# Kernel tuning notes

Hardware: AMD Instinct MI355X
Metric: run time of the kernel (lower is better)

Reference implementation:

```python
import jax, jax.numpy as jnp
import numpy as np

N_NODES = 50000
N_EDGES = 800000
IN_CH = 128
OUT_CH = 32
HEADS = 4
NEG_SLOPE = 0.2


def setup_inputs() -> dict:
    key = jax.random.key(0)
    k_feat, k_src, k_dst, k_w, k_a = jax.random.split(key, 5)
    feat = jax.random.normal(k_feat, (N_NODES, IN_CH), dtype=jnp.float32)
    src = jax.random.randint(k_src, (N_EDGES,), 0, N_NODES, dtype=jnp.int64)
    dst = jax.random.randint(k_dst, (N_EDGES,), 0, N_NODES, dtype=jnp.int64)
    # forward removes self-loops then re-adds them; build inputs with no self-loops
    dst = jnp.where(src == dst, (dst + 1) % N_NODES, dst)
    edge_index = jnp.stack([src, dst])  # [2, E]
    # glorot init, matching reset_parameters
    def glorot(k, shape):
        stdv = np.sqrt(6.0 / (shape[-2] + shape[-1]))
        return jax.random.uniform(k, shape, jnp.float32, -stdv, stdv)
    weight = glorot(k_w, (IN_CH, HEADS * OUT_CH))
    att = glorot(k_a, (1, HEADS, 2 * OUT_CH))
    bias = jnp.zeros((HEADS * OUT_CH,), dtype=jnp.float32)
    return {"feat": feat, "edge_index": edge_index, "weight": weight, "att": att, "bias": bias}


def reference(feat, edge_index, weight, att, bias):
    N = feat.shape[0]
    # add self-loops (inputs are constructed self-loop free)
    loop = jnp.arange(N, dtype=edge_index.dtype)
    ei = jnp.concatenate([edge_index, jnp.stack([loop, loop])], axis=1)
    src, dst = ei[0], ei[1]

    x = (feat @ weight).reshape(N, HEADS, OUT_CH)  # [N,H,C]
    x_i = x[dst]  # dst features, [E,H,C]
    x_j = x[src]  # src features, [E,H,C]

    # GAT attention: sum over concat([x_i, x_j]) * att
    alpha = jnp.sum(jnp.concatenate([x_i, x_j], axis=-1) * att, axis=-1)  # [E,H]
    alpha = jax.nn.leaky_relu(alpha, NEG_SLOPE)

    # scatter softmax normalized per src node (edge_index[0]), as in the original code
    amax = jax.ops.segment_max(alpha, src, num_segments=N)  # every node is a src (self-loops)
    amax = jax.lax.stop_gradient(amax)
    ex = jnp.exp(alpha - amax[src])
    esum = jax.ops.segment_sum(ex, src, num_segments=N)
    alpha = ex / (esum[src] + 1e-16)  # [E,H]

    neighbor = x_j * alpha[:, :, None]  # [E,H,C]
    out = jax.ops.segment_sum(neighbor, dst, num_segments=N)  # sum-aggregate into dst
    out = out.reshape(N, HEADS * OUT_CH) + bias  # concat heads + bias
    return out
```

## Files before the change

### kernel.cpp

```cpp
#include <hip/hip_runtime.h>
#include <hip/hip_bf16.h>

#define N_NODES 50000
#define E_EDGES 800000
#define ET (E_EDGES + N_NODES)
#define HEADS 4
#define HC 128
#define NEG_SLOPE 0.2f
#define SCAN_B 256
#define NBLK ((N_NODES + SCAN_B - 1) / SCAN_B)

__device__ __forceinline__ unsigned short f2bf(float f) {
    unsigned u = __float_as_uint(f);
    unsigned r = u + 0x7FFFu + ((u >> 16) & 1u);
    return (unsigned short)(r >> 16);
}

__global__ __launch_bounds__(256)
void gemm_kernel(const float* __restrict__ feat, const float* __restrict__ weight,
                 const float* __restrict__ att,
                 unsigned short* __restrict__ xb,
                 float* __restrict__ a_i, float* __restrict__ a_j)
{
    __shared__ float sA[32][68];
    __shared__ float sB[32][132];
    const int t = threadIdx.x;
    const int row0 = blockIdx.x * 64;
    const int rg = t >> 4;
    const int cg = t & 15;

    float acc[4][8];
#pragma unroll
    for (int i = 0; i < 4; i++)
#pragma unroll
        for (int j = 0; j < 8; j++) acc[i][j] = 0.f;

    for (int kc = 0; kc < 128; kc += 32) {
        __syncthreads();
#pragma unroll
        for (int q = 0; q < 2; q++) {
            int qi = t + q * 256;
            int row = qi >> 3;
            int kq = qi & 7;
            int grow = row0 + row;
            float4 v = make_float4(0.f, 0.f, 0.f, 0.f);
            if (grow < N_NODES)
                v = *(const float4*)&feat[grow * 128 + kc + kq * 4];
            sA[kq * 4 + 0][row] = v.x; sA[kq * 4 + 1][row] = v.y;
            sA[kq * 4 + 2][row] = v.z; sA[kq * 4 + 3][row] = v.w;
        }
#pragma unroll
        for (int q = 0; q < 4; q++) {
            int qi = t + q * 256;
            int k = qi >> 5;
            int cq = qi & 31;
            float4 v = *(const float4*)&weight[(kc + k) * 128 + cq * 4];
            *(float4*)&sB[k][cq * 4] = v;
        }
        __syncthreads();
#pragma unroll 4
        for (int k = 0; k < 32; k++) {
            float4 a0 = *(const float4*)&sA[k][4 * rg];
            float4 b0 = *(const float4*)&sB[k][4 * cg];
            float4 b1 = *(const float4*)&sB[k][64 + 4 * cg];
#define FMA_ROW(r, ar) \
            acc[r][0] = fmaf(ar, b0.x, acc[r][0]); \
            acc[r][1] = fmaf(ar, b0.y, acc[r][1]); \
            acc[r][2] = fmaf(ar, b0.z, acc[r][2]); \
            acc[r][3] = fmaf(ar, b0.w, acc[r][3]); \
            acc[r][4] = fmaf(ar, b1.x, acc[r][4]); \
            acc[r][5] = fmaf(ar, b1.y, acc[r][5]); \
            acc[r][6] = fmaf(ar, b1.z, acc[r][6]); \
            acc[r][7] = fmaf(ar, b1.w, acc[r][7]);
            FMA_ROW(0, a0.x)
            FMA_ROW(1, a0.y)
            FMA_ROW(2, a0.z)
            FMA_ROW(3, a0.w)
#undef FMA_ROW
        }
    }

    const int h0 = cg >> 3;
    const int cih = (4 * cg) & 31;
    float ai_c[2][4], aj_c[2][4];
#pragma unroll
    for (int g = 0; g < 2; g++) {
        int h = h0 + g * 2;
#pragma unroll
        for (int j = 0; j < 4; j++) {
            ai_c[g][j] = att[h * 64 + cih + j];
            aj_c[g][j] = att[h * 64 + 32 + cih + j];
        }
    }
#pragma unroll
    for (int i = 0; i < 4; i++) {
        int row = row0 + 4 * rg + i;
        if (row >= N_NODES) continue;
        unsigned p0 = (unsigned)f2bf(acc[i][0]) | ((unsigned)f2bf(acc[i][1]) << 16);
        unsigned p1 = (unsigned)f2bf(acc[i][2]) | ((unsigned)f2bf(acc[i][3]) << 16);
        unsigned p2 = (unsigned)f2bf(acc[i][4]) | ((unsigned)f2bf(acc[i][5]) << 16);
        unsigned p3 = (unsigned)f2bf(acc[i][6]) | ((unsigned)f2bf(acc[i][7]) << 16);
        uint2 q0; q0.x = p0; q0.y = p1;
        uint2 q1; q1.x = p2; q1.y = p3;
        *(uint2*)&xb[row * 128 + 4 * cg] = q0;
        *(uint2*)&xb[row * 128 + 64 + 4 * cg] = q1;

        float pi0 = 0.f, pj0 = 0.f, pi1 = 0.f, pj1 = 0.f;
#pragma unroll
        for (int j = 0; j < 4; j++) {
            pi0 = fmaf(acc[i][j], ai_c[0][j], pi0);
            pj0 = fmaf(acc[i][j], aj_c[0][j], pj0);
            pi1 = fmaf(acc[i][4 + j], ai_c[1][j], pi1);
            pj1 = fmaf(acc[i][4 + j], aj_c[1][j], pj1);
        }
#pragma unroll
        for (int m = 1; m <= 4; m <<= 1) {
            pi0 += __shfl_xor(pi0, m, 64);
            pj0 += __shfl_xor(pj0, m, 64);
            pi1 += __shfl_xor(pi1, m, 64);
            pj1 += __shfl_xor(pj1, m, 64);
        }
        if ((cg & 7) == 0) {
            a_i[row * 4 + h0]     = pi0;
            a_i[row * 4 + h0 + 2] = pi1;
            a_j[row * 4 + h0]     = pj0;
            a_j[row * 4 + h0 + 2] = pj1;
        }
    }
}

__global__ __launch_bounds__(256)
void rank_pass(const int* __restrict__ ei, int* __restrict__ deg_s,
               int* __restrict__ deg_d, unsigned short* __restrict__ rank_s,
               unsigned short* __restrict__ rank_d)
{
    int e = blockIdx.x * 256 + threadIdx.x;
    if (e >= ET) return;
    int s, d;
    if (e < E_EDGES) { s = ei[e]; d = ei[E_EDGES + e]; }
    else { s = d = e - E_EDGES; }
    rank_s[e] = (unsigned short)atomicAdd(&deg_s[s], 1);
    rank_d[e] = (unsigned short)atomicAdd(&deg_d[d], 1);
}

__global__ __launch_bounds__(SCAN_B)
void partial_kernel(const int* __restrict__ deg_s, const int* __restrict__ deg_d,
                    int* __restrict__ partials)
{
    __shared__ int wsum[4];
    int half = (blockIdx.x < NBLK) ? 0 : 1;
    int blk = half ? (blockIdx.x - NBLK) : blockIdx.x;
    const int* deg = half ? deg_d : deg_s;
    int idx = blk * SCAN_B + threadIdx.x;
    int v = (idx < N_NODES) ? deg[idx] : 0;
#pragma unroll
    for (int m = 1; m < 64; m <<= 1) v += __shfl_xor(v, m, 64);
    int lane = threadIdx.x & 63, wid = threadIdx.x >> 6;
    if (lane == 0) wsum[wid] = v;
    __syncthreads();
    if (threadIdx.x == 0)
        partials[blockIdx.x] = wsum[0] + wsum[1] + wsum[2] + wsum[3];
}

__global__ __launch_bounds__(512)
void scanp_kernel(int* __restrict__ partials, int* __restrict__ off_s,
                  int* __restrict__ off_d)
{
    __shared__ int sh[512];
    int t = threadIdx.x;
    int hf = t & 255;
    int v = 0;
    if (t < 256)      v = (hf < NBLK) ? partials[hf] : 0;
    else              v = (hf < NBLK) ? partials[NBLK + hf] : 0;
    sh[t] = v;
    __syncthreads();
    for (int dlt = 1; dlt < 256; dlt <<= 1) {
        int u = (hf >= dlt) ? sh[t - dlt] : 0;
        __syncthreads();
        sh[t] += u;
        __syncthreads();
    }
    int excl = (hf == 0) ? 0 : sh[t - 1];
    if (t < 256) { if (hf < NBLK) partials[hf] = excl; }
    else         { if (hf < NBLK) partials[NBLK + hf] = excl; }
    if (t == NBLK - 1)       off_s[N_NODES] = sh[t];
    if (t == 256 + NBLK - 1) off_d[N_NODES] = sh[t];
}

__global__ __launch_bounds__(SCAN_B)
void final_kernel(const int* __restrict__ deg_s, const int* __restrict__ deg_d,
                  const int* __restrict__ partials,
                  int* __restrict__ off_s, int* __restrict__ off_d)
{
    __shared__ int wsum[4];
    int half = (blockIdx.x < NBLK) ? 0 : 1;
    int blk = half ? (blockIdx.x - NBLK) : blockIdx.x;
    const int* deg = half ? deg_d : deg_s;
    int* off = half ? off_d : off_s;
    int idx = blk * SCAN_B + threadIdx.x;
    int val = (idx < N_NODES) ? deg[idx] : 0;
    int lane = threadIdx.x & 63, wid = threadIdx.x >> 6;
    int x = val;
#pragma unroll
    for (int dlt = 1; dlt < 64; dlt <<= 1) {
        int y = __shfl_up(x, dlt, 64);
        if (lane >= dlt) x += y;
    }
    if (lane == 63) wsum[wid] = x;
    __syncthreads();
    int woff = 0;
    for (int w = 0; w < wid; w++) woff += wsum[w];
    int excl = x - val + woff + partials[blockIdx.x];
    if (idx < N_NODES) off[idx] = excl;
}

__global__ __launch_bounds__(256)
void place_kernel(const int* __restrict__ ei, const int* __restrict__ off_s,
                  const int* __restrict__ off_d,
                  const unsigned short* __restrict__ rank_s,
                  const unsigned short* __restrict__ rank_d,
                  int* __restrict__ adj_dst, int* __restrict__ adj_src)
{
    int e = blockIdx.x * 256 + threadIdx.x;
    if (e >= ET) return;
    int s, d;
    if (e < E_EDGES) { s = ei[e]; d = ei[E_EDGES + e]; }
    else { s = d = e - E_EDGES; }
    adj_dst[off_s[s] + rank_s[e]] = d;
    adj_src[off_d[d] + rank_d[e]] = s;
}

__global__ __launch_bounds__(256)
void esum_kernel(const int* __restrict__ off_s, const int* __restrict__ adj_dst,
                 const float* __restrict__ a_i, const float* __restrict__ a_j,
                 float* __restrict__ esum)
{
    int tid = blockIdx.x * 256 + threadIdx.x;
    int node = tid >> 2;
    if (node >= N_NODES) return;
    int h = tid & 3;
    int start = off_s[node], end = off_s[node + 1];
    float ajh = a_j[node * 4 + h];
    float acc = 0.f;
    int s_cur[4];
#pragma unroll
    for (int k = 0; k < 4; k++)
        s_cur[k] = (start + k < end) ? adj_dst[start + k] : 0;
    for (int i0 = start; i0 < end; i0 += 4) {
        int i1 = i0 + 4;
        int s_nxt[4];
#pragma unroll
        for (int k = 0; k < 4; k++)
            s_nxt[k] = (i1 + k < end) ? adj_dst[i1 + k] : 0;
        float aiv[4];
#pragma unroll
        for (int k = 0; k < 4; k++)
            aiv[k] = a_i[s_cur[k] * 4 + h];
#pragma unroll
        for (int k = 0; k < 4; k++) {
            if (i0 + k < end) {
                float al = aiv[k] + ajh;
                al = al > 0.f ? al : NEG_SLOPE * al;
                acc += __expf(al);
            }
        }
#pragma unroll
        for (int k = 0; k < 4; k++) s_cur[k] = s_nxt[k];
    }
    esum[node * 4 + h] = acc;
}

__global__ __launch_bounds__(256)
void coef_kernel(const int* __restrict__ off_d, const int* __restrict__ adj_src,
                 const float* __restrict__ a_i, const float* __restrict__ a_j,
                 const float* __restrict__ esum, float* __restrict__ coef)
{
    int tid = blockIdx.x * 256 + threadIdx.x;
    int node = tid >> 2;
    if (node >= N_NODES) return;
    int h = tid & 3;
    int start = off_d[node], end = off_d[node + 1];
    float aih = a_i[node * 4 + h];
    int s_cur[4];
#pragma unroll
    for (int k = 0; k < 4; k++)
        s_cur[k] = (start + k < end) ? adj_src[start + k] : 0;
    for (int i0 = start; i0 < end; i0 += 4) {
        int i1 = i0 + 4;
        int s_nxt[4];
#pragma unroll
        for (int k = 0; k < 4; k++)
            s_nxt[k] = (i1 + k < end) ? adj_src[i1 + k] : 0;
        float ajv[4], esv[4];
#pragma unroll
        for (int k = 0; k < 4; k++) {
            ajv[k] = a_j[s_cur[k] * 4 + h];
            esv[k] = esum[s_cur[k] * 4 + h];
        }
#pragma unroll
        for (int k = 0; k < 4; k++) {
            if (i0 + k < end) {
                float al = aih + ajv[k];
                al = al > 0.f ? al : NEG_SLOPE * al;
                coef[(i0 + k) * 4 + h] = __expf(al) / (esv[k] + 1e-16f);
            }
        }
#pragma unroll
        for (int k = 0; k < 4; k++) s_cur[k] = s_nxt[k];
    }
}

__global__ __launch_bounds__(256)
void aggregate(const int* __restrict__ off, const int* __restrict__ srcsorted,
               const float* __restrict__ coef, const unsigned* __restrict__ xb32,
               const float* __restrict__ bias, float* __restrict__ out)
{
    int node = blockIdx.x * 4 + (threadIdx.x >> 6);
    if (node >= N_NODES) return;
    int lane = threadIdx.x & 63;
    int h = lane >> 4;
    int start = off[node], end = off[node + 1];
    float acc0 = 0.f, acc1 = 0.f;

    int s_cur[4]; float c_cur[4];
#pragma unroll
    for (int k = 0; k < 4; k++) {
        bool v = (start + k < end);
        s_cur[k] = v ? srcsorted[start + k] : 0;
        c_cur[k] = v ? coef[(start + k) * 4 + h] : 0.f;
    }
    for (int i0 = start; i0 < end; i0 += 4) {
        int i1 = i0 + 4;
        int s_nxt[4]; float c_nxt[4];
#pragma unroll
        for (int k = 0; k < 4; k++) {
            bool v = (i1 + k < end);
            s_nxt[k] = v ? srcsorted[i1 + k] : 0;
            c_nxt[k] = v ? coef[(i1 + k) * 4 + h] : 0.f;
        }
        unsigned xp[4];
#pragma unroll
        for (int k = 0; k < 4; k++)
            xp[k] = xb32[s_cur[k] * 64 + lane];
#pragma unroll
        for (int k = 0; k < 4; k++) {
            float x0 = __uint_as_float(xp[k] << 16);
            float x1 = __uint_as_float(xp[k] & 0xFFFF0000u);
            acc0 = fmaf(x0, c_cur[k], acc0);
            acc1 = fmaf(x1, c_cur[k], acc1);
        }
#pragma unroll
        for (int k = 0; k < 4; k++) { s_cur[k] = s_nxt[k]; c_cur[k] = c_nxt[k]; }
    }
    float2 o;
    o.x = acc0 + bias[2 * lane];
    o.y = acc1 + bias[2 * lane + 1];
    *(float2*)&out[node * 128 + 2 * lane] = o;
}

extern "C" void kernel_launch(void* const* d_in, const int* in_sizes, int n_in,
                              void* d_out, int out_size, void* d_ws, size_t ws_size,
                              hipStream_t stream)
{
    const float* feat   = (const float*)d_in[0];
    const int*   ei     = (const int*)d_in[1];
    const float* weight = (const float*)d_in[2];
    const float* att    = (const float*)d_in[3];
    const float* bias   = (const float*)d_in[4];
    float* out = (float*)d_out;
    char* ws = (char*)d_ws;

    unsigned short* rank_s = (unsigned short*)ws;
    unsigned short* rank_d = (unsigned short*)(ws + 1700000);
    unsigned short* xb = (unsigned short*)ws;
    float* a_i   = (float*)(ws + 12800000);
    float* a_j   = (float*)(ws + 13600000);
    float* esum  = (float*)(ws + 14400000);
    int*   deg_s = (int*)(ws + 15200000);
    int*   deg_d = (int*)(ws + 15400000);
    int*   off_s = (int*)(ws + 15600000);
    int*   off_d = (int*)(ws + 15800016);
    int*   adj_dst = (int*)(ws + 16000032);
    int*   adj_src = (int*)(ws + 19400032);
    int*   partials = (int*)(ws + 22800032);
    float* coef  = (float*)(ws + 22801600);

    hipMemsetAsync(ws + 15200000, 0, 400000, stream);

    rank_pass<<<(ET + 255) / 256, 256, 0, stream>>>(ei, deg_s, deg_d, rank_s, rank_d);
    partial_kernel<<<2 * NBLK, SCAN_B, 0, stream>>>(deg_s, deg_d, partials);
    scanp_kernel<<<1, 512, 0, stream>>>(partials, off_s, off_d);
    final_kernel<<<2 * NBLK, SCAN_B, 0, stream>>>(deg_s, deg_d, partials, off_s, off_d);
    place_kernel<<<(ET + 255) / 256, 256, 0, stream>>>(ei, off_s, off_d, rank_s, rank_d,
                                                       adj_dst, adj_src);
    gemm_kernel<<<(N_NODES + 63) / 64, 256, 0, stream>>>(feat, weight, att, xb, a_i, a_j);
    esum_kernel<<<(4 * N_NODES + 255) / 256, 256, 0, stream>>>(off_s, adj_dst, a_i, a_j, esum);
    coef_kernel<<<(4 * N_NODES + 255) / 256, 256, 0, stream>>>(off_d, adj_src, a_i, a_j,
                                                               esum, coef);
    aggregate<<<(N_NODES + 3) / 4, 256, 0, stream>>>(off_d, adj_src, coef,
                                                     (const unsigned*)xb, bias, out);
}
```

Baseline: 279.3 us.

## Replace global-atomic degree counting with LDS-partitioned node-range counting

Swaps the per-edge global atomic degree/rank pass for 32 blocks that each own a contiguous node range held in shared memory. Every block streams the full edge list and does LDS atomics only for nodes in its range, and self-loops are pre-counted by initialising counts to 1. This removes the memset and the contended global atomics, but each block rereads all edges and only 32 blocks run, so parallelism is low.

```diff
diff --git a/kernel.cpp b/kernel.cpp
--- a/kernel.cpp
+++ b/kernel.cpp
@@ -9,6 +9,8 @@
 #define NEG_SLOPE 0.2f
 #define SCAN_B 256
 #define NBLK ((N_NODES + SCAN_B - 1) / SCAN_B)
+#define RB 32
+#define NPR ((N_NODES + RB - 1) / RB)
 
 __device__ __forceinline__ unsigned short f2bf(float f) {
     unsigned u = __float_as_uint(f);
@@ -130,17 +132,44 @@
 }
 
 __global__ __launch_bounds__(256)
-void rank_pass(const int* __restrict__ ei, int* __restrict__ deg_s,
-               int* __restrict__ deg_d, unsigned short* __restrict__ rank_s,
-               unsigned short* __restrict__ rank_d)
-{
-    int e = blockIdx.x * 256 + threadIdx.x;
-    if (e >= ET) return;
-    int s, d;
-    if (e < E_EDGES) { s = ei[e]; d = ei[E_EDGES + e]; }
-    else { s = d = e - E_EDGES; }
-    rank_s[e] = (unsigned short)atomicAdd(&deg_s[s], 1);
-    rank_d[e] = (unsigned short)atomicAdd(&deg_d[d], 1);
+void count_rank(const int* __restrict__ ei,
+                unsigned short* __restrict__ rank_s,
+                unsigned short* __restrict__ rank_d,
+                int* __restrict__ deg_s, int* __restrict__ deg_d)
+{
+    __shared__ int cs[NPR];
+    __shared__ int cd[NPR];
+    const int t = threadIdx.x;
+    const int base = blockIdx.x * NPR;
+    const int lim = min(NPR, N_NODES - base);
+
+    for (int i = t; i < NPR; i += 256) { cs[i] = 1; cd[i] = 1; }
+    for (int i = t; i < lim; i += 256) {
+        rank_s[E_EDGES + base + i] = 0;
+        rank_d[E_EDGES + base + i] = 0;
+    }
+    __syncthreads();
+
+    for (int e = t * 4; e < E_EDGES; e += 1024) {
+        int4 s4 = *(const int4*)&ei[e];
+        int4 d4 = *(const int4*)&ei[E_EDGES + e];
+        int sv[4] = {s4.x, s4.y, s4.z, s4.w};
+        int dv[4] = {d4.x, d4.y, d4.z, d4.w};
+#pragma unroll
+        for (int k = 0; k < 4; k++) {
+            int so = sv[k] - base;
+            if ((unsigned)so < (unsigned)lim)
+                rank_s[e + k] = (unsigned short)atomicAdd(&cs[so], 1);
+            int dd = dv[k] - base;
+            if ((unsigned)dd < (unsigned)lim)
+                rank_d[e + k] = (unsigned short)atomicAdd(&cd[dd], 1);
+        }
+    }
+    __syncthreads();
+    for (int i = t; i < lim; i += 256) {
+        deg_s[base + i] = cs[i];
+        deg_d[base + i] = cd[i];
+    }
 }
 
 __global__ __launch_bounds__(SCAN_B)
@@ -385,9 +414,7 @@
     int*   partials = (int*)(ws + 22800032);
     float* coef  = (float*)(ws + 22801600);
 
-    hipMemsetAsync(ws + 15200000, 0, 400000, stream);
-
-    rank_pass<<<(ET + 255) / 256, 256, 0, stream>>>(ei, deg_s, deg_d, rank_s, rank_d);
+    count_rank<<<RB, 256, 0, stream>>>(ei, rank_s, rank_d, deg_s, deg_d);
     partial_kernel<<<2 * NBLK, SCAN_B, 0, stream>>>(deg_s, deg_d, partials);
     scanp_kernel<<<1, 512, 0, stream>>>(partials, off_s, off_d);
     final_kernel<<<2 * NBLK, SCAN_B, 0, stream>>>(deg_s, deg_d, partials, off_s, off_d);
```

New measurement: 777.5 us. 178% more time.
